# Optimization experiments

Measured on AMD Instinct MI355X. Metric: run time of the kernel, lower is better.

Reference implementation:

```python
import jax, jax.numpy as jnp
import numpy as np

B, S, D = 2, 2048, 2048
H, KV, HD = 32, 8, 64
REP = H // KV


def rotate_half(t):
    t1, t2 = t[..., : t.shape[-1] // 2], t[..., t.shape[-1] // 2 :]
    return jnp.concatenate((-t2, t1), axis=-1)


def setup_inputs() -> dict:
    key = jax.random.key(0)
    kx, kq, kk, kv, ko = jax.random.split(key, 5)
    x = jax.random.normal(kx, (B, S, D), dtype=jnp.float32) * 0.02
    # RoPE tables: shape [S, HD//2]; forward concatenates [cos, cos] to reach HD
    inv_freq = 1.0 / (10000.0 ** (np.arange(0, HD, 2, dtype=np.float32) / HD))
    freqs = np.outer(np.arange(S, dtype=np.float32), inv_freq)
    cos = jnp.asarray(np.cos(freqs), dtype=jnp.float32)
    sin = jnp.asarray(np.sin(freqs), dtype=jnp.float32)
    # causal additive mask [1,1,S,S]
    causal = np.tril(np.ones((S, S), dtype=bool))
    mask = jnp.asarray(np.where(causal, 0.0, -1e9).astype(np.float32))[None, None]
    s = 0.02
    wq = jax.random.normal(kq, (H * HD, D), dtype=jnp.float32) * s
    wk = jax.random.normal(kk, (KV * HD, D), dtype=jnp.float32) * s
    wv = jax.random.normal(kv, (KV * HD, D), dtype=jnp.float32) * s
    wo = jax.random.normal(ko, (D, H * HD), dtype=jnp.float32) * s
    return {"x": x, "cos": cos, "sin": sin, "mask": mask,
            "wq": wq, "wk": wk, "wv": wv, "wo": wo}


def reference(x, cos, sin, mask, wq, wk, wv, wo):
    b, s, d = x.shape
    # QKV projections (Linear with bias=False: x @ W^T)
    q = jnp.einsum("bsd,ed->bse", x, wq).reshape(b, s, H, HD)
    k = jnp.einsum("bsd,ed->bse", x, wk).reshape(b, s, KV, HD)
    v = jnp.einsum("bsd,ed->bse", x, wv).reshape(b, s, KV, HD)
    # RoPE: cos/sin [S, HD//2] -> [1, S, 1, HD]
    cc = jnp.concatenate([cos[:s], cos[:s]], axis=-1)[None, :, None, :]
    ss = jnp.concatenate([sin[:s], sin[:s]], axis=-1)[None, :, None, :]
    q = q * cc + rotate_half(q) * ss
    k = k * cc + rotate_half(k) * ss
    # GQA: group q heads by kv head (implicit broadcast instead of repeat_kv)
    q = q.transpose(0, 2, 1, 3).reshape(b, KV, REP, s, HD)  # [B,KV,REP,S,HD]
    k = k.transpose(0, 2, 1, 3)                              # [B,KV,S,HD]
    v = v.transpose(0, 2, 1, 3)                              # [B,KV,S,HD]
    scores = jnp.einsum("bkrqd,bksd->bkrqs", q, k) / np.sqrt(HD)
    scores = scores + mask[:, :, None, :, :]  # broadcast over rep dim
    probs = jax.nn.softmax(scores.astype(jnp.float32), axis=-1).astype(q.dtype)
    out = jnp.einsum("bkrqs,bksd->bkrqd", probs, v)
    out = out.transpose(0, 3, 1, 2, 4).reshape(b, s, H * HD)  # [B,S,H*HD]
    return jnp.einsum("bse,de->bsd", out, wo)
```

## Files before the change

kernel.cpp:

```cpp
#include <hip/hip_runtime.h>
#include <stdint.h>

#define DEV __device__ __forceinline__

typedef __bf16 bf16;
typedef __bf16 bf16x8 __attribute__((ext_vector_type(8)));
typedef __bf16 bf16x4v __attribute__((ext_vector_type(4)));
typedef float f32x4 __attribute__((ext_vector_type(4)));
typedef float f32x16 __attribute__((ext_vector_type(16)));
typedef int int2v __attribute__((ext_vector_type(2)));

constexpr int Bb = 2, Ss = 2048, Dd = 2048, Hh = 32, KVh = 8, HDd = 64;
constexpr int Mm = Bb * Ss;
constexpr int EQ = Hh * HDd;
constexpr int EKV = KVh * HDd;
constexpr int Ee = EQ + 2 * EKV;

DEV void gload16(const void* g, void* l) {
  __builtin_amdgcn_global_load_lds((const __attribute__((address_space(1))) uint32_t*)g,
                                   (__attribute__((address_space(3))) uint32_t*)l, 16, 0, 0);
}

#if __has_builtin(__builtin_amdgcn_exp2f)
DEV float exp2_fast(float x) { return __builtin_amdgcn_exp2f(x); }
#else
DEV float exp2_fast(float x) {
  float r;
  asm("v_exp_f32 %0, %1\n\ts_nop 0" : "=v"(r) : "v"(x));
  return r;
}
#endif
DEV uint32_t cvtpk(float lo, float hi) {
  uint32_t w;
  asm("v_cvt_pk_bf16_f32 %0, %1, %2" : "=v"(w) : "v"(lo), "v"(hi));
  return w;
}
DEV int2v pswap(uint32_t a, uint32_t b) {
  return __builtin_amdgcn_permlane32_swap((int)a, (int)b, false, false);
}
DEV float fu(uint32_t u) { union { uint32_t u; float f; } c; c.u = u; return c.f; }
DEV uint32_t uf(float f) { union { float f; uint32_t u; } c; c.f = f; return c.u; }

__global__ void cvt_kernel(const float* __restrict__ x, const float* __restrict__ wq,
                           const float* __restrict__ wk, const float* __restrict__ wv,
                           const float* __restrict__ wo,
                           bf16* __restrict__ xb, bf16* __restrict__ wqkvb,
                           bf16* __restrict__ wob) {
  const long NX = (long)Mm * Dd;
  const long NQ = (long)EQ * Dd;
  const long NK = (long)EKV * Dd;
  const long NO = (long)Dd * EQ;
  const long total4 = (NX + NQ + 2 * NK + NO) / 4;
  for (long i = (long)blockIdx.x * blockDim.x + threadIdx.x; i < total4;
       i += (long)gridDim.x * blockDim.x) {
    long e = i * 4;
    const float* src; bf16* dst;
    if (e < NX)                { src = x + e;                       dst = xb + e; }
    else if (e < NX + NQ)      { long o = e - NX;                   src = wq + o; dst = wqkvb + o; }
    else if (e < NX + NQ + NK) { long o = e - NX - NQ;              src = wk + o; dst = wqkvb + NQ + o; }
    else if (e < NX + NQ + 2*NK){ long o = e - NX - NQ - NK;        src = wv + o; dst = wqkvb + NQ + NK + o; }
    else                       { long o = e - NX - NQ - 2*NK;       src = wo + o; dst = wob + o; }
    float4 v = *(const float4*)src;
    bf16x4v b;
    b.x = (bf16)v.x; b.y = (bf16)v.y; b.z = (bf16)v.z; b.w = (bf16)v.w;
    *(bf16x4v*)dst = b;
  }
}

template <int BN, bool OUT_BF16>
__global__ __launch_bounds__(512, 1)
void gemm_bt(const bf16* __restrict__ A, const bf16* __restrict__ Bt,
             float* __restrict__ Cf, bf16* __restrict__ Cb,
             int Mn, int Nn, int Kn) {
  constexpr int NJ = BN / 64;
  constexpr int RB = BN / 4;
  constexpr int NB0 = (BN == 192) ? 2 : 1;
  __shared__ __align__(16) bf16 As[2][256 * 64];
  __shared__ __align__(16) bf16 Bs[2][BN * 64];
  const int tid = threadIdx.x, wid = tid >> 6, lane = tid & 63;
  const int g = lane >> 4, c = lane & 15;
  const int wm = wid >> 2, wn = wid & 3;

  const int xcd = (int)blockIdx.x & 7;
  const int idx = (int)blockIdx.x >> 3;
  const int bi = (xcd >> 1) * 4 + (idx >> 3);
  const int bj = (xcd & 1) * 8 + (idx & 7);
  const long arow0 = (long)bi * 256, brow0 = (long)bj * BN;

  const int srow = tid >> 3, schk = tid & 7;
  const int cs = schk ^ (srow & 7);

  f32x4 acc[8][NJ] = {};

#pragma unroll
  for (int it = 0; it < 4; ++it)
    gload16(A + (arow0 + it * 64 + srow) * Kn + cs * 8,
            (char*)&As[0][0] + it * 8192 + tid * 16);
#pragma unroll
  for (int q = 0; q < NJ; ++q)
    gload16(Bt + (brow0 + q * 64 + srow) * Kn + cs * 8,
            (char*)&Bs[0][0] + q * 8192 + tid * 16);
  __syncthreads();

  const int NT = Kn >> 6;
  for (int kt = 0; kt < NT; ++kt) {
    const char* pa = (const char*)&As[kt & 1][0];
    const char* pb = (const char*)&Bs[kt & 1][0];
    char* na = (char*)&As[(kt + 1) & 1][0];
    char* nb = (char*)&Bs[(kt + 1) & 1][0];
    const bool more = (kt + 1 < NT);
    bf16x8 bfr[NJ][2];

#pragma unroll
    for (int p = 0; p < 2; ++p) {
      bf16x8 af[4][2];
#pragma unroll
      for (int i2 = 0; i2 < 4; ++i2)
#pragma unroll
        for (int ks = 0; ks < 2; ++ks) {
          int r = wm * 128 + (4 * p + i2) * 16 + c;
          af[i2][ks] = *(const bf16x8*)(pa + r * 128 + (((ks * 4 + g) ^ (r & 7)) << 4));
        }
      if (p == 0) {
#pragma unroll
        for (int j = 0; j < NJ; ++j)
#pragma unroll
          for (int ks = 0; ks < 2; ++ks) {
            int r = wn * RB + j * 16 + c;
            bfr[j][ks] = *(const bf16x8*)(pb + r * 128 + (((ks * 4 + g) ^ (r & 7)) << 4));
          }
      }
      if (more) {
        if (p == 0) {
#pragma unroll
          for (int bq = 0; bq < NB0; ++bq)
            gload16(Bt + (brow0 + bq * 64 + srow) * Kn + (kt + 1) * 64 + cs * 8,
                    nb + bq * 8192 + tid * 16);
        } else {
#pragma unroll
          for (int bq = NB0; bq < NJ; ++bq)
            gload16(Bt + (brow0 + bq * 64 + srow) * Kn + (kt + 1) * 64 + cs * 8,
                    nb + bq * 8192 + tid * 16);
        }
#pragma unroll
        for (int aq = 0; aq < 2; ++aq) {
          int qn = 2 * p + aq;
          gload16(A + (arow0 + qn * 64 + srow) * Kn + (kt + 1) * 64 + cs * 8,
                  na + qn * 8192 + tid * 16);
        }
      }
      __builtin_amdgcn_s_barrier();
      asm volatile("s_waitcnt lgkmcnt(0)" ::: "memory");
      __builtin_amdgcn_s_setprio(1);
#pragma unroll
      for (int i2 = 0; i2 < 4; ++i2)
#pragma unroll
        for (int j = 0; j < NJ; ++j)
#pragma unroll
          for (int ks = 0; ks < 2; ++ks)
            acc[4 * p + i2][j] =
                __builtin_amdgcn_mfma_f32_16x16x32_bf16(af[i2][ks], bfr[j][ks],
                                                        acc[4 * p + i2][j], 0, 0, 0);
      __builtin_amdgcn_s_setprio(0);
      if (p == 0) {
        if (BN == 192) asm volatile("s_waitcnt vmcnt(4)" ::: "memory");
        else           asm volatile("s_waitcnt vmcnt(3)" ::: "memory");
        __builtin_amdgcn_s_barrier();
      }
    }
    asm volatile("s_waitcnt vmcnt(1)" ::: "memory");
    __builtin_amdgcn_s_barrier();
  }

#pragma unroll
  for (int i = 0; i < 8; ++i)
#pragma unroll
    for (int j = 0; j < NJ; ++j)
#pragma unroll
      for (int r = 0; r < 4; ++r) {
        long row = arow0 + wm * 128 + i * 16 + 4 * g + r;
        long col = brow0 + wn * RB + j * 16 + c;
        if (OUT_BF16) Cb[row * Nn + col] = (bf16)acc[i][j][r];
        else          Cf[row * Nn + col] = acc[i][j][r];
      }
}

__global__ void kv_prep_kernel(const bf16* __restrict__ qkv, const float* __restrict__ cosT,
                               const float* __restrict__ sinT, bf16* __restrict__ kout,
                               bf16* __restrict__ vtb) {
  if (blockIdx.x < 512) {
    __shared__ __align__(16) unsigned short tile[64][72];
    int blk = blockIdx.x;
    int st = blk & 31, kvh = (blk >> 5) & 7, b = blk >> 8;
    int s0 = st * 64;
    int t = threadIdx.x;
#pragma unroll
    for (int rep = 0; rep < 2; ++rep) {
      int idx = t + rep * 256;
      int r = idx >> 3, cb = idx & 7;
      const bf16* src = qkv + ((long)(b * Ss + s0 + r)) * Ee + EQ + EKV + kvh * 64 + cb * 8;
      *(uint4*)&tile[r][cb * 8] = *(const uint4*)src;
    }
    __syncthreads();
#pragma unroll
    for (int rep = 0; rep < 2; ++rep) {
      int idx = t + rep * 256;
      int dd = idx >> 3, scb = idx & 7;
      union { unsigned short u[8]; uint4 v; } pk;
#pragma unroll
      for (int j = 0; j < 8; ++j) pk.u[j] = tile[scb * 8 + j][dd];
      long dst = ((long)((b * KVh + kvh) * 64 + dd)) * Ss + s0 + scb * 8;
      *(uint4*)&vtb[dst] = pk.v;
    }
  } else {
    int tid = (int)(blockIdx.x - 512) * blockDim.x + threadIdx.x;
    int d = tid & 31;
    int h = (tid >> 5) & (KVh - 1);
    int m = tid >> 8;
    if (m >= Mm) return;
    int s = m & (Ss - 1), b = m >> 11;
    float lo = (float)qkv[(long)m * Ee + EQ + h * 64 + d];
    float hi = (float)qkv[(long)m * Ee + EQ + h * 64 + d + 32];
    float cs = cosT[s * 32 + d], sn = sinT[s * 32 + d];
    long base = (((long)(b * KVh + h)) * Ss + s) * 64;
    kout[base + d]      = (bf16)(lo * cs - hi * sn);
    kout[base + d + 32] = (bf16)(hi * cs + lo * sn);
  }
}

__global__ __launch_bounds__(512)
void attn_kernel(const bf16* __restrict__ qkv, const float* __restrict__ cosT,
                 const float* __restrict__ sinT, const bf16* __restrict__ k,
                 const bf16* __restrict__ vt, bf16* __restrict__ o) {
  __shared__ __align__(16) bf16 Kt[2][2][64 * 64];
  __shared__ __align__(16) bf16 Vt[2][2][64 * 64];
  constexpr float SCL = 0.18033688f;

  const int tid = threadIdx.x, qw = tid >> 6, lane = tid & 63;
  const int ql = lane & 31, hi = lane >> 5;
  const int g6 = (int)(blockIdx.x >> 6);
  const int qt = (g6 < 4) ? (7 - g6) : (g6 - 4);
  const int bh = blockIdx.x & 63;
  const int b = bh >> 5, h = bh & 31;
  const int kvh = h >> 2;
  const int q0 = qt * 256;
  const int qw_q0 = q0 + qw * 32;

  const bf16* kbase = k + ((long)(b * KVh + kvh)) * Ss * 64;
  const bf16* vbase = vt + ((long)(b * KVh + kvh)) * 64 * Ss;

  const int srow = tid >> 3, scb = tid & 7;
  const int scbs = scb ^ (srow & 7);
  const int sdst = tid * 16;

  bf16x8 qf[4];
  {
    const int s_row = q0 + qw * 32 + ql;
    const bf16* qrow = qkv + ((long)(b * Ss + s_row)) * Ee + h * 64 + 8 * hi;
    bf16x8 qraw[4];
#pragma unroll
    for (int ks = 0; ks < 4; ++ks) qraw[ks] = *(const bf16x8*)(qrow + 16 * ks);
    float cs8[2][8], sn8[2][8];
#pragma unroll
    for (int ks2 = 0; ks2 < 2; ++ks2) {
      const float* cp = cosT + s_row * 32 + 16 * ks2 + 8 * hi;
      const float* sp = sinT + s_row * 32 + 16 * ks2 + 8 * hi;
      *(float4*)&cs8[ks2][0] = *(const float4*)cp;
      *(float4*)&cs8[ks2][4] = *(const float4*)(cp + 4);
      *(float4*)&sn8[ks2][0] = *(const float4*)sp;
      *(float4*)&sn8[ks2][4] = *(const float4*)(sp + 4);
    }
#pragma unroll
    for (int ks2 = 0; ks2 < 2; ++ks2)
#pragma unroll
      for (int j = 0; j < 8; ++j) {
        float lo = (float)qraw[ks2][j], hv = (float)qraw[ks2 + 2][j];
        qf[ks2][j]     = (bf16)((lo * cs8[ks2][j] - hv * sn8[ks2][j]) * SCL);
        qf[ks2 + 2][j] = (bf16)((hv * cs8[ks2][j] + lo * sn8[ks2][j]) * SCL);
      }
  }

  bf16x8 bones;
#pragma unroll
  for (int j = 0; j < 8; ++j) bones[j] = (bf16)1.0f;

  gload16(kbase + (long)srow * 64 + scbs * 8, (char*)&Kt[0][0][0] + sdst);
  gload16(kbase + ((long)64 + srow) * 64 + scbs * 8, (char*)&Kt[0][1][0] + sdst);
  gload16(vbase + (long)srow * Ss + scbs * 8, (char*)&Vt[0][0][0] + sdst);
  gload16(vbase + (long)srow * Ss + 64 + scbs * 8, (char*)&Vt[0][1][0] + sdst);
  __syncthreads();

  f32x16 Oacc0 = {}, Oacc1 = {}, lacc = {};
  const int qa = qw_q0 + ql;
  const int nt = 4 * qt + 4;
  const int ntp = nt >> 1;
  const int tdiag = qw_q0 >> 6;

  int cur = 0;
  for (int pp = 0; pp < ntp; ++pp) {
    if (pp + 1 < ntp) {
      int nb = cur ^ 1;
      long t0 = (long)(2 * pp + 2) * 64;
      gload16(kbase + (t0 + srow) * 64 + scbs * 8, (char*)&Kt[nb][0][0] + sdst);
      gload16(kbase + (t0 + 64 + srow) * 64 + scbs * 8, (char*)&Kt[nb][1][0] + sdst);
      gload16(vbase + (long)srow * Ss + t0 + scbs * 8, (char*)&Vt[nb][0][0] + sdst);
      gload16(vbase + (long)srow * Ss + t0 + 64 + scbs * 8, (char*)&Vt[nb][1][0] + sdst);
    }

#pragma unroll
    for (int half = 0; half < 2; ++half) {
      const int t = 2 * pp + half;
      if (64 * t < qw_q0 + 32) {
        f32x16 s0 = {}, s1 = {};
        const char* kt = (const char*)&Kt[cur][half][0];
#pragma unroll
        for (int ks = 0; ks < 4; ++ks) {
          int chk = ((2 * ks + hi) ^ (ql & 7)) << 4;
          bf16x8 kf0 = *(const bf16x8*)(kt + ql * 128 + chk);
          bf16x8 kf1 = *(const bf16x8*)(kt + (32 + ql) * 128 + chk);
          s0 = __builtin_amdgcn_mfma_f32_32x32x16_bf16(kf0, qf[ks], s0, 0, 0, 0);
          s1 = __builtin_amdgcn_mfma_f32_32x32x16_bf16(kf1, qf[ks], s1, 0, 0, 0);
        }

        if (t == tdiag) {
#pragma unroll
          for (int r = 0; r < 16; ++r) {
            int kv0 = t * 64 + (r & 3) + 8 * (r >> 2) + 4 * hi;
            if (kv0 > qa)      s0[r] = -1e30f;
            if (kv0 + 32 > qa) s1[r] = -1e30f;
          }
        }

#pragma unroll
        for (int r = 0; r < 16; ++r) {
          s0[r] = exp2_fast(s0[r]);
          s1[r] = exp2_fast(s1[r]);
        }

        const char* vtb0 = (const char*)&Vt[cur][half][0];
#pragma unroll
        for (int ks = 0; ks < 4; ++ks) {
          uint32_t pk01, pk23, pk45, pk67;
          if (ks < 2) {
            const int rb = (ks & 1) * 8;
            pk01 = cvtpk(s0[rb + 0], s0[rb + 1]);
            pk23 = cvtpk(s0[rb + 2], s0[rb + 3]);
            pk45 = cvtpk(s0[rb + 4], s0[rb + 5]);
            pk67 = cvtpk(s0[rb + 6], s0[rb + 7]);
          } else {
            const int rb = (ks & 1) * 8;
            pk01 = cvtpk(s1[rb + 0], s1[rb + 1]);
            pk23 = cvtpk(s1[rb + 2], s1[rb + 3]);
            pk45 = cvtpk(s1[rb + 4], s1[rb + 5]);
            pk67 = cvtpk(s1[rb + 6], s1[rb + 7]);
          }
          int2v w02 = pswap(pk01, pk45);
          int2v w13 = pswap(pk23, pk67);
          union { uint32_t u[4]; bf16x8 v; } pa;
          pa.u[0] = (uint32_t)w02.x; pa.u[1] = (uint32_t)w13.x;
          pa.u[2] = (uint32_t)w02.y; pa.u[3] = (uint32_t)w13.y;

          int chk = ((2 * ks + hi) ^ (ql & 7)) << 4;
          bf16x8 vf0 = *(const bf16x8*)(vtb0 + ql * 128 + chk);
          bf16x8 vf1 = *(const bf16x8*)(vtb0 + (32 + ql) * 128 + chk);
          Oacc0 = __builtin_amdgcn_mfma_f32_32x32x16_bf16(pa.v, vf0, Oacc0, 0, 0, 0);
          Oacc1 = __builtin_amdgcn_mfma_f32_32x32x16_bf16(pa.v, vf1, Oacc1, 0, 0, 0);
          lacc  = __builtin_amdgcn_mfma_f32_32x32x16_bf16(pa.v, bones, lacc, 0, 0, 0);
        }
      }
    }

    __syncthreads();
    cur ^= 1;
  }

#pragma unroll
  for (int r = 0; r < 16; ++r) {
    int qrow = (r & 3) + 8 * (r >> 2) + 4 * hi;
    float li = 1.0f / lacc[r];
    long orow = (long)b * Ss + q0 + 32 * qw + qrow;
    o[orow * EQ + h * 64 + ql]      = (bf16)(Oacc0[r] * li);
    o[orow * EQ + h * 64 + 32 + ql] = (bf16)(Oacc1[r] * li);
  }
}

extern "C" void kernel_launch(void* const* d_in, const int* in_sizes, int n_in,
                              void* d_out, int out_size, void* d_ws, size_t ws_size,
                              hipStream_t stream) {
  const float* x    = (const float*)d_in[0];
  const float* cosT = (const float*)d_in[1];
  const float* sinT = (const float*)d_in[2];
  const float* wq   = (const float*)d_in[4];
  const float* wk   = (const float*)d_in[5];
  const float* wv   = (const float*)d_in[6];
  const float* wo   = (const float*)d_in[7];

  if (ws_size < 104857600u) return;

  char* ws = (char*)d_ws;
  bf16* xb    = (bf16*)(ws + 0);
  bf16* wqkvb = (bf16*)(ws + 16777216);
  bf16* wob   = (bf16*)(ws + 29360128);
  bf16* qkvb  = (bf16*)(ws + 37748736);
  bf16* kb    = (bf16*)(ws + 79691776);
  bf16* vtb   = (bf16*)(ws + 83886080);
  bf16* attnb = (bf16*)(ws + 88080384);
  float* outp = (float*)d_out;

  cvt_kernel<<<dim3(2048), dim3(256), 0, stream>>>(x, wq, wk, wv, wo, xb, wqkvb, wob);
  gemm_bt<192, true><<<dim3((Mm / 256) * (Ee / 192)), dim3(512), 0, stream>>>(
      xb, wqkvb, (float*)nullptr, qkvb, Mm, Ee, Dd);
  kv_prep_kernel<<<dim3(512 + (Mm * KVh * 32) / 256), dim3(256), 0, stream>>>(
      qkvb, cosT, sinT, kb, vtb);
  attn_kernel<<<dim3(512), dim3(512), 0, stream>>>(qkvb, cosT, sinT, kb, vtb, attnb);
  gemm_bt<128, false><<<dim3((Mm / 256) * (EQ / 128)), dim3(512), 0, stream>>>(
      attnb, wob, outp, (bf16*)nullptr, Mm, EQ, EQ);
}
```

Baseline: 162.5 us.

## Shrink attention blocks to 128 query rows with 4 waves and single-tile KV steps

```diff
diff --git a/kernel.cpp b/kernel.cpp
--- a/kernel.cpp
+++ b/kernel.cpp
@@ -228,30 +228,30 @@
   }
 }
 
-__global__ __launch_bounds__(512)
+__global__ __launch_bounds__(256)
 void attn_kernel(const bf16* __restrict__ qkv, const float* __restrict__ cosT,
                  const float* __restrict__ sinT, const bf16* __restrict__ k,
                  const bf16* __restrict__ vt, bf16* __restrict__ o) {
-  __shared__ __align__(16) bf16 Kt[2][2][64 * 64];
-  __shared__ __align__(16) bf16 Vt[2][2][64 * 64];
+  __shared__ __align__(16) bf16 Kt[2][64 * 64];
+  __shared__ __align__(16) bf16 Vt[2][64 * 64];
   constexpr float SCL = 0.18033688f;
 
   const int tid = threadIdx.x, qw = tid >> 6, lane = tid & 63;
   const int ql = lane & 31, hi = lane >> 5;
-  const int g6 = (int)(blockIdx.x >> 6);
-  const int qt = (g6 < 4) ? (7 - g6) : (g6 - 4);
+  const int qi = (int)(blockIdx.x >> 6);
+  const int r4 = qi & 3, c4 = qi >> 2;
+  const int qt = (c4 == 0) ? (15 - r4) : (c4 == 1) ? (8 + r4) : (c4 == 2) ? (7 - r4) : r4;
   const int bh = blockIdx.x & 63;
   const int b = bh >> 5, h = bh & 31;
   const int kvh = h >> 2;
-  const int q0 = qt * 256;
+  const int q0 = qt * 128;
   const int qw_q0 = q0 + qw * 32;
 
   const bf16* kbase = k + ((long)(b * KVh + kvh)) * Ss * 64;
   const bf16* vbase = vt + ((long)(b * KVh + kvh)) * 64 * Ss;
 
-  const int srow = tid >> 3, scb = tid & 7;
-  const int scbs = scb ^ (srow & 7);
-  const int sdst = tid * 16;
+  const int srow0 = tid >> 3, scb = tid & 7;
+  const int sdst0 = tid * 16;
 
   bf16x8 qf[4];
   {
@@ -284,89 +284,90 @@
 #pragma unroll
   for (int j = 0; j < 8; ++j) bones[j] = (bf16)1.0f;
 
-  gload16(kbase + (long)srow * 64 + scbs * 8, (char*)&Kt[0][0][0] + sdst);
-  gload16(kbase + ((long)64 + srow) * 64 + scbs * 8, (char*)&Kt[0][1][0] + sdst);
-  gload16(vbase + (long)srow * Ss + scbs * 8, (char*)&Vt[0][0][0] + sdst);
-  gload16(vbase + (long)srow * Ss + 64 + scbs * 8, (char*)&Vt[0][1][0] + sdst);
+#pragma unroll
+  for (int it = 0; it < 2; ++it) {
+    int row = srow0 + 32 * it;
+    int cbs = scb ^ (row & 7);
+    gload16(kbase + (long)row * 64 + cbs * 8, (char*)&Kt[0][0] + sdst0 + it * 4096);
+    gload16(vbase + (long)row * Ss + cbs * 8, (char*)&Vt[0][0] + sdst0 + it * 4096);
+  }
   __syncthreads();
 
   f32x16 Oacc0 = {}, Oacc1 = {}, lacc = {};
   const int qa = qw_q0 + ql;
-  const int nt = 4 * qt + 4;
-  const int ntp = nt >> 1;
+  const int nt = 2 * qt + 2;
   const int tdiag = qw_q0 >> 6;
 
   int cur = 0;
-  for (int pp = 0; pp < ntp; ++pp) {
-    if (pp + 1 < ntp) {
+  for (int t = 0; t < nt; ++t) {
+    if (t + 1 < nt) {
       int nb = cur ^ 1;
-      long t0 = (long)(2 * pp + 2) * 64;
-      gload16(kbase + (t0 + srow) * 64 + scbs * 8, (char*)&Kt[nb][0][0] + sdst);
-      gload16(kbase + (t0 + 64 + srow) * 64 + scbs * 8, (char*)&Kt[nb][1][0] + sdst);
-      gload16(vbase + (long)srow * Ss + t0 + scbs * 8, (char*)&Vt[nb][0][0] + sdst);
-      gload16(vbase + (long)srow * Ss + t0 + 64 + scbs * 8, (char*)&Vt[nb][1][0] + sdst);
-    }
-
-#pragma unroll
-    for (int half = 0; half < 2; ++half) {
-      const int t = 2 * pp + half;
-      if (64 * t < qw_q0 + 32) {
-        f32x16 s0 = {}, s1 = {};
-        const char* kt = (const char*)&Kt[cur][half][0];
-#pragma unroll
-        for (int ks = 0; ks < 4; ++ks) {
-          int chk = ((2 * ks + hi) ^ (ql & 7)) << 4;
-          bf16x8 kf0 = *(const bf16x8*)(kt + ql * 128 + chk);
-          bf16x8 kf1 = *(const bf16x8*)(kt + (32 + ql) * 128 + chk);
-          s0 = __builtin_amdgcn_mfma_f32_32x32x16_bf16(kf0, qf[ks], s0, 0, 0, 0);
-          s1 = __builtin_amdgcn_mfma_f32_32x32x16_bf16(kf1, qf[ks], s1, 0, 0, 0);
+      long t0 = (long)(t + 1) * 64;
+#pragma unroll
+      for (int it = 0; it < 2; ++it) {
+        int row = srow0 + 32 * it;
+        int cbs = scb ^ (row & 7);
+        gload16(kbase + (t0 + row) * 64 + cbs * 8, (char*)&Kt[nb][0] + sdst0 + it * 4096);
+        gload16(vbase + (long)row * Ss + t0 + cbs * 8, (char*)&Vt[nb][0] + sdst0 + it * 4096);
+      }
+    }
+
+    if (64 * t < qw_q0 + 32) {
+      f32x16 s0 = {}, s1 = {};
+      const char* kt = (const char*)&Kt[cur][0];
+#pragma unroll
+      for (int ks = 0; ks < 4; ++ks) {
+        int chk = ((2 * ks + hi) ^ (ql & 7)) << 4;
+        bf16x8 kf0 = *(const bf16x8*)(kt + ql * 128 + chk);
+        bf16x8 kf1 = *(const bf16x8*)(kt + (32 + ql) * 128 + chk);
+        s0 = __builtin_amdgcn_mfma_f32_32x32x16_bf16(kf0, qf[ks], s0, 0, 0, 0);
+        s1 = __builtin_amdgcn_mfma_f32_32x32x16_bf16(kf1, qf[ks], s1, 0, 0, 0);
+      }
+
+      if (t == tdiag) {
+#pragma unroll
+        for (int r = 0; r < 16; ++r) {
+          int kv0 = t * 64 + (r & 3) + 8 * (r >> 2) + 4 * hi;
+          if (kv0 > qa)      s0[r] = -1e30f;
+          if (kv0 + 32 > qa) s1[r] = -1e30f;
         }
-
-        if (t == tdiag) {
-#pragma unroll
-          for (int r = 0; r < 16; ++r) {
-            int kv0 = t * 64 + (r & 3) + 8 * (r >> 2) + 4 * hi;
-            if (kv0 > qa)      s0[r] = -1e30f;
-            if (kv0 + 32 > qa) s1[r] = -1e30f;
-          }
+      }
+
+#pragma unroll
+      for (int r = 0; r < 16; ++r) {
+        s0[r] = exp2_fast(s0[r]);
+        s1[r] = exp2_fast(s1[r]);
+      }
+
+      const char* vtb0 = (const char*)&Vt[cur][0];
+#pragma unroll
+      for (int ks = 0; ks < 4; ++ks) {
+        uint32_t pk01, pk23, pk45, pk67;
+        if (ks < 2) {
+          const int rb = (ks & 1) * 8;
+          pk01 = cvtpk(s0[rb + 0], s0[rb + 1]);
+          pk23 = cvtpk(s0[rb + 2], s0[rb + 3]);
+          pk45 = cvtpk(s0[rb + 4], s0[rb + 5]);
+          pk67 = cvtpk(s0[rb + 6], s0[rb + 7]);
+        } else {
+          const int rb = (ks & 1) * 8;
+          pk01 = cvtpk(s1[rb + 0], s1[rb + 1]);
+          pk23 = cvtpk(s1[rb + 2], s1[rb + 3]);
+          pk45 = cvtpk(s1[rb + 4], s1[rb + 5]);
+          pk67 = cvtpk(s1[rb + 6], s1[rb + 7]);
         }
-
-#pragma unroll
-        for (int r = 0; r < 16; ++r) {
-          s0[r] = exp2_fast(s0[r]);
-          s1[r] = exp2_fast(s1[r]);
-        }
-
-        const char* vtb0 = (const char*)&Vt[cur][half][0];
-#pragma unroll
-        for (int ks = 0; ks < 4; ++ks) {
-          uint32_t pk01, pk23, pk45, pk67;
-          if (ks < 2) {
-            const int rb = (ks & 1) * 8;
-            pk01 = cvtpk(s0[rb + 0], s0[rb + 1]);
-            pk23 = cvtpk(s0[rb + 2], s0[rb + 3]);
-            pk45 = cvtpk(s0[rb + 4], s0[rb + 5]);
-            pk67 = cvtpk(s0[rb + 6], s0[rb + 7]);
-          } else {
-            const int rb = (ks & 1) * 8;
-            pk01 = cvtpk(s1[rb + 0], s1[rb + 1]);
-            pk23 = cvtpk(s1[rb + 2], s1[rb + 3]);
-            pk45 = cvtpk(s1[rb + 4], s1[rb + 5]);
-            pk67 = cvtpk(s1[rb + 6], s1[rb + 7]);
-          }
-          int2v w02 = pswap(pk01, pk45);
-          int2v w13 = pswap(pk23, pk67);
-          union { uint32_t u[4]; bf16x8 v; } pa;
-          pa.u[0] = (uint32_t)w02.x; pa.u[1] = (uint32_t)w13.x;
-          pa.u[2] = (uint32_t)w02.y; pa.u[3] = (uint32_t)w13.y;
-
-          int chk = ((2 * ks + hi) ^ (ql & 7)) << 4;
-          bf16x8 vf0 = *(const bf16x8*)(vtb0 + ql * 128 + chk);
-          bf16x8 vf1 = *(const bf16x8*)(vtb0 + (32 + ql) * 128 + chk);
-          Oacc0 = __builtin_amdgcn_mfma_f32_32x32x16_bf16(pa.v, vf0, Oacc0, 0, 0, 0);
-          Oacc1 = __builtin_amdgcn_mfma_f32_32x32x16_bf16(pa.v, vf1, Oacc1, 0, 0, 0);
-          lacc  = __builtin_amdgcn_mfma_f32_32x32x16_bf16(pa.v, bones, lacc, 0, 0, 0);
-        }
+        int2v w02 = pswap(pk01, pk45);
+        int2v w13 = pswap(pk23, pk67);
+        union { uint32_t u[4]; bf16x8 v; } pa;
+        pa.u[0] = (uint32_t)w02.x; pa.u[1] = (uint32_t)w13.x;
+        pa.u[2] = (uint32_t)w02.y; pa.u[3] = (uint32_t)w13.y;
+
+        int chk = ((2 * ks + hi) ^ (ql & 7)) << 4;
+        bf16x8 vf0 = *(const bf16x8*)(vtb0 + ql * 128 + chk);
+        bf16x8 vf1 = *(const bf16x8*)(vtb0 + (32 + ql) * 128 + chk);
+        Oacc0 = __builtin_amdgcn_mfma_f32_32x32x16_bf16(pa.v, vf0, Oacc0, 0, 0, 0);
+        Oacc1 = __builtin_amdgcn_mfma_f32_32x32x16_bf16(pa.v, vf1, Oacc1, 0, 0, 0);
+        lacc  = __builtin_amdgcn_mfma_f32_32x32x16_bf16(pa.v, bones, lacc, 0, 0, 0);
       }
     }
 
@@ -412,7 +413,7 @@
       xb, wqkvb, (float*)nullptr, qkvb, Mm, Ee, Dd);
   kv_prep_kernel<<<dim3(512 + (Mm * KVh * 32) / 256), dim3(256), 0, stream>>>(
       qkvb, cosT, sinT, kb, vtb);
-  attn_kernel<<<dim3(512), dim3(512), 0, stream>>>(qkvb, cosT, sinT, kb, vtb, attnb);
+  attn_kernel<<<dim3(1024), dim3(256), 0, stream>>>(qkvb, cosT, sinT, kb, vtb, attnb);
   gemm_bt<128, false><<<dim3((Mm / 256) * (EQ / 128)), dim3(512), 0, stream>>>(
       attnb, wob, outp, (bf16*)nullptr, Mm, EQ, EQ);
 }
```

Result: slower. 170.8 us (+5.1%).
